# Kernel tuning notes

Measured on AMD Instinct MI355X. Metric: run time of the kernel, lower is better.

Reference implementation:

```python
import jax, jax.numpy as jnp
import numpy as np

H = 16  # n_heads (from init_kwargs)


def l2norm(x, eps=1e-6):
    return x * jax.lax.rsqrt(jnp.sum(x * x, axis=-1, keepdims=True) + eps)


def causal_conv1d(x, w, b):
    # depthwise causal conv: x (B,T,D), w (D,k), b (D,). Matches torch
    # Conv1d(d,d,k,groups=d,padding=k-1) followed by [:, :, :T] truncation.
    T = x.shape[1]
    k = w.shape[1]
    xp = jnp.pad(x, ((0, 0), (k - 1, 0), (0, 0)))
    y = b
    for j in range(k):  # k=4 taps, fixed small loop
        y = y + xp[:, j:j + T, :] * w[:, j]
    return y


def setup_inputs():
    key = jax.random.key(0)
    ks = jax.random.split(key, 16)
    B, T, D, kc = 2, 2048, 1024, 4
    d = D // H
    s = 1.0 / np.sqrt(D)
    return {
        "x": jax.random.normal(ks[0], (B, T, D), jnp.float32),
        "Wq": jax.random.normal(ks[1], (D, D), jnp.float32) * s,
        "Wk": jax.random.normal(ks[2], (D, D), jnp.float32) * s,
        "Wv": jax.random.normal(ks[3], (D, D), jnp.float32) * s,
        "Wo": jax.random.normal(ks[4], (D, D), jnp.float32) * s,
        "Wg": jax.random.normal(ks[5], (D, D), jnp.float32) * s,
        "Wb": jax.random.normal(ks[6], (D, H), jnp.float32) * s,
        "cq_w": jax.random.normal(ks[7], (D, kc), jnp.float32) * 0.3,
        "cq_b": jax.random.normal(ks[8], (D,), jnp.float32) * 0.1,
        "ck_w": jax.random.normal(ks[9], (D, kc), jnp.float32) * 0.3,
        "ck_b": jax.random.normal(ks[10], (D,), jnp.float32) * 0.1,
        "cv_w": jax.random.normal(ks[11], (D, kc), jnp.float32) * 0.3,
        "cv_b": jax.random.normal(ks[12], (D,), jnp.float32) * 0.1,
        "nw": jnp.ones((d,), jnp.float32),
    }


def reference(x, Wq, Wk, Wv, Wo, Wg, Wb, cq_w, cq_b, ck_w, ck_b, cv_w, cv_b, nw):
    B, T, D = x.shape
    d = D // H
    q = l2norm(jax.nn.silu(causal_conv1d(x @ Wq, cq_w, cq_b)).reshape(B, T, H, d))
    q = q / jnp.sqrt(jnp.asarray(d, x.dtype))
    k = l2norm(jax.nn.silu(causal_conv1d(x @ Wk, ck_w, ck_b)).reshape(B, T, H, d))
    v = jax.nn.silu(causal_conv1d(x @ Wv, cv_w, cv_b)).reshape(B, T, H, d)
    gate = (x @ Wg).reshape(B, T, H, d)
    beta = jax.nn.sigmoid(x @ Wb)[..., None]  # (B,T,H,1)

    def step(S, qkvb):
        q_t, k_t, v_t, b_t = qkvb  # (B,H,d), (B,H,d), (B,H,d), (B,H,1)
        err = (v_t - jnp.einsum('bhk,bhkv->bhv', k_t, S)) * b_t
        S = S + jnp.einsum('bhk,bhv->bhkv', k_t, err)
        o_t = jnp.einsum('bhk,bhkv->bhv', q_t, S)
        return S, o_t

    S0 = jnp.zeros((B, H, d, d), x.dtype)
    xs = (q.transpose(1, 0, 2, 3), k.transpose(1, 0, 2, 3),
          v.transpose(1, 0, 2, 3), beta.transpose(1, 0, 2, 3))
    _, oT = jax.lax.scan(step, S0, xs)
    o = oT.transpose(1, 0, 2, 3)  # (B,T,H,d)
    # RMSNorm over head_dim
    o = o * jax.lax.rsqrt(jnp.mean(o * o, axis=-1, keepdims=True) + 1e-5) * nw
    o = o * jax.nn.silu(gate)
    return o.reshape(B, T, D) @ Wo
```

## Files before the change

kernel.cpp:

```cpp
#include <hip/hip_runtime.h>
#include <hip/hip_bf16.h>

typedef __attribute__((ext_vector_type(8))) short short8;
typedef __attribute__((ext_vector_type(4))) float f32x4;

#define TSEQ 2048
#define DMODEL 1024
#define NH 16
#define HD 64
#define PLANE 4194304

__device__ __forceinline__ ushort f2bf(float f) {
    union { float f; unsigned int u; } c; c.f = f;
    unsigned int u = c.u + 0x7fffu + ((c.u >> 16) & 1u);
    return (ushort)(u >> 16);
}

__device__ __forceinline__ float bf2f(ushort u) {
    union { unsigned int i; float f; } c; c.i = ((unsigned int)u) << 16;
    return c.f;
}

__device__ __forceinline__ void split2(float x, ushort& h, ushort& l) {
    h = f2bf(x);
    float r = x - bf2f(h);
    l = f2bf(r);
}

__device__ __forceinline__ float silu_f(float y) {
    return y / (1.f + __expf(-y));
}

__device__ __forceinline__ void gl_lds16(const float* g, float* l) {
    __builtin_amdgcn_global_load_lds(
        (__attribute__((address_space(1))) void*)g,
        (__attribute__((address_space(3))) void*)l, 16, 0, 0);
}
__device__ __forceinline__ void gl_lds16u(const ushort* g, ushort* l) {
    __builtin_amdgcn_global_load_lds(
        (__attribute__((address_space(1))) void*)g,
        (__attribute__((address_space(3))) void*)l, 16, 0, 0);
}

__global__ void gdn_cvt_x(const float* __restrict__ x, ushort* __restrict__ xb) {
    int i = blockIdx.x * 256 + threadIdx.x;
    float4 v = ((const float4*)x)[i];
    ushort4 o;
    o.x = f2bf(v.x); o.y = f2bf(v.y); o.z = f2bf(v.z); o.w = f2bf(v.w);
    ((ushort4*)xb)[i] = o;
}

__global__ void gdn_cvt_w(const float* __restrict__ Wq, const float* __restrict__ Wk,
                          const float* __restrict__ Wv, const float* __restrict__ Wg,
                          const float* __restrict__ Wo, ushort* __restrict__ wt) {
    __shared__ float tile[32][33];
    int z = blockIdx.z;
    const float* W = (z == 0) ? Wq : (z == 1) ? Wk : (z == 2) ? Wv : (z == 3) ? Wg : Wo;
    int n0 = blockIdx.x * 32, k0 = blockIdx.y * 32;
    int tx = threadIdx.x, ty = threadIdx.y;
    #pragma unroll
    for (int j = 0; j < 32; j += 8)
        tile[ty + j][tx] = W[(size_t)(k0 + ty + j) * DMODEL + n0 + tx];
    __syncthreads();
    ushort* o = wt + (size_t)z * DMODEL * DMODEL;
    #pragma unroll
    for (int j = 0; j < 32; j += 8)
        o[(size_t)(n0 + ty + j) * DMODEL + k0 + tx] = f2bf(tile[tx][ty + j]);
}

__global__ void gdn_beta(const float* __restrict__ x, const float* __restrict__ Wb,
                         float* __restrict__ betaT) {
    __shared__ float xs[16][DMODEL];
    int tid = threadIdx.x;
    int m0 = blockIdx.x * 16;
    #pragma unroll
    for (int i = 0; i < 16; i++) {
        int idx = i * 256 + tid;
        int row = idx >> 8, c4 = idx & 255;
        *(float4*)&xs[row][c4 * 4] =
            *(const float4*)&x[(size_t)(m0 + row) * DMODEL + c4 * 4];
    }
    __syncthreads();
    int h = tid & 15, mi = tid >> 4;
    float acc = 0.f;
    for (int k = 0; k < DMODEL; ++k)
        acc += xs[mi][k] * Wb[k * NH + h];
    int m = m0 + mi;
    int b = m >> 11, t = m & (TSEQ - 1);
    betaT[((b * NH + h) << 11) + t] = 1.f / (1.f + __expf(-acc));
}

#define BK 32
__global__ __launch_bounds__(256) void gdn_gemm(const ushort* __restrict__ A,
                                                const ushort* __restrict__ Bt,
                                                float* __restrict__ outF,
                                                size_t planeStride) {
    __shared__ ushort As[128 * BK];
    __shared__ ushort Bs[128 * BK];
    int tid = threadIdx.x;
    int lane = tid & 63, wid = tid >> 6;
    int wm = wid & 1, wn = wid >> 1;
    int l15 = lane & 15, quad = lane >> 4;
    int bm = blockIdx.x, bn = blockIdx.y;
    const int K = DMODEL;

    int e0 = wid, e1 = wid + 4;
    int srow0 = e0 * 16 + (lane >> 2), srow1 = e1 * 16 + (lane >> 2);
    int scol = (lane & 3) * 8;
    const ushort* Ag0 = A + (size_t)(bm * 128 + srow0) * K + scol;
    const ushort* Ag1 = A + (size_t)(bm * 128 + srow1) * K + scol;
    const ushort* Bg0 = Bt + (size_t)(bn * 128 + srow0) * K + scol;
    const ushort* Bg1 = Bt + (size_t)(bn * 128 + srow1) * K + scol;
    ushort* Al0 = As + e0 * 512;
    ushort* Al1 = As + e1 * 512;
    ushort* Bl0 = Bs + e0 * 512;
    ushort* Bl1 = Bs + e1 * 512;

    f32x4 acc[4][4];
    #pragma unroll
    for (int i = 0; i < 4; i++)
        #pragma unroll
        for (int j = 0; j < 4; j++)
            acc[i][j] = (f32x4){0.f, 0.f, 0.f, 0.f};

    for (int kt = 0; kt < K; kt += BK) {
        __syncthreads();
        gl_lds16u(Ag0 + kt, Al0);
        gl_lds16u(Ag1 + kt, Al1);
        gl_lds16u(Bg0 + kt, Bl0);
        gl_lds16u(Bg1 + kt, Bl1);
        __syncthreads();
        short8 af[4], bf[4];
        #pragma unroll
        for (int i = 0; i < 4; i++) {
            af[i] = *(const short8*)&As[(wm * 64 + i * 16 + l15) * BK + quad * 8];
            bf[i] = *(const short8*)&Bs[(wn * 64 + i * 16 + l15) * BK + quad * 8];
        }
        #pragma unroll
        for (int mt = 0; mt < 4; mt++)
            #pragma unroll
            for (int nt = 0; nt < 4; nt++)
                acc[mt][nt] = __builtin_amdgcn_mfma_f32_16x16x32_bf16(
                    af[mt], bf[nt], acc[mt][nt], 0, 0, 0);
    }

    #pragma unroll
    for (int mt = 0; mt < 4; mt++)
        #pragma unroll
        for (int nt = 0; nt < 4; nt++)
            #pragma unroll
            for (int r = 0; r < 4; r++) {
                int row = bm * 128 + wm * 64 + mt * 16 + quad * 4 + r;
                int col = bn * 128 + wn * 64 + nt * 16 + l15;
                outF[(size_t)(col >> 10) * planeStride + (size_t)row * 1024 + (col & 1023)]
                    = acc[mt][nt][r];
            }
}

__global__ __launch_bounds__(512, 2) void gdn_gemm256(const ushort* __restrict__ A,
                                                      const ushort* __restrict__ Bt,
                                                      float* __restrict__ outF,
                                                      size_t planeStride) {
    __shared__ ushort As[3][256 * BK];
    __shared__ ushort Bs[3][256 * BK];
    int tid = threadIdx.x;
    int lane = tid & 63, wid = tid >> 6;
    int wm = wid >> 2, wn = wid & 3;
    int l15 = lane & 15, quad = lane >> 4;
    int bm = blockIdx.x, bn = blockIdx.y;
    const int K = DMODEL;

    int e0 = wid * 2, e1 = wid * 2 + 1;
    int srow0 = e0 * 16 + (lane >> 2), srow1 = e1 * 16 + (lane >> 2);
    int scol = (lane & 3) * 8;
    const ushort* Ag0 = A + (size_t)(bm * 256 + srow0) * K + scol;
    const ushort* Ag1 = A + (size_t)(bm * 256 + srow1) * K + scol;
    const ushort* Bg0 = Bt + (size_t)(bn * 256 + srow0) * K + scol;
    const ushort* Bg1 = Bt + (size_t)(bn * 256 + srow1) * K + scol;

    f32x4 acc[8][4];
    #pragma unroll
    for (int i = 0; i < 8; i++)
        #pragma unroll
        for (int j = 0; j < 4; j++)
            acc[i][j] = (f32x4){0.f, 0.f, 0.f, 0.f};

    #pragma unroll
    for (int t = 0; t < 2; t++) {
        gl_lds16u(Ag0 + t * BK, &As[t][e0 * 512]);
        gl_lds16u(Ag1 + t * BK, &As[t][e1 * 512]);
        gl_lds16u(Bg0 + t * BK, &Bs[t][e0 * 512]);
        gl_lds16u(Bg1 + t * BK, &Bs[t][e1 * 512]);
    }
    asm volatile("s_waitcnt vmcnt(4)" ::: "memory");
    __builtin_amdgcn_s_barrier();

    #pragma unroll 1
    for (int c = 0; c < 32; ++c) {
        if (c + 2 < 32) {
            int s2 = (c + 2) % 3;
            int kt2 = (c + 2) * BK;
            gl_lds16u(Ag0 + kt2, &As[s2][e0 * 512]);
            gl_lds16u(Ag1 + kt2, &As[s2][e1 * 512]);
            gl_lds16u(Bg0 + kt2, &Bs[s2][e0 * 512]);
            gl_lds16u(Bg1 + kt2, &Bs[s2][e1 * 512]);
        }
        int cs = c % 3;
        short8 af[8], bf[4];
        #pragma unroll
        for (int mi = 0; mi < 8; mi++)
            af[mi] = *(const short8*)&As[cs][(wm * 128 + mi * 16 + l15) * BK + quad * 8];
        #pragma unroll
        for (int ni = 0; ni < 4; ni++)
            bf[ni] = *(const short8*)&Bs[cs][(wn * 64 + ni * 16 + l15) * BK + quad * 8];
        #pragma unroll
        for (int mi = 0; mi < 8; mi++)
            #pragma unroll
            for (int ni = 0; ni < 4; ni++)
                acc[mi][ni] = __builtin_amdgcn_mfma_f32_16x16x32_bf16(
                    af[mi], bf[ni], acc[mi][ni], 0, 0, 0);
        if (c < 30) {
            asm volatile("s_waitcnt vmcnt(4)" ::: "memory");
            __builtin_amdgcn_s_barrier();
        } else if (c == 30) {
            asm volatile("s_waitcnt vmcnt(0)" ::: "memory");
            __builtin_amdgcn_s_barrier();
        }
    }

    #pragma unroll
    for (int mi = 0; mi < 8; mi++)
        #pragma unroll
        for (int ni = 0; ni < 4; ni++)
            #pragma unroll
            for (int r = 0; r < 4; r++) {
                int row = bm * 256 + wm * 128 + mi * 16 + quad * 4 + r;
                int col = bn * 256 + wn * 64 + ni * 16 + l15;
                outF[(size_t)(col >> 10) * planeStride + (size_t)row * 1024 + (col & 1023)]
                    = acc[mi][ni][r];
            }
}

__global__ void gdn_conv(const float* __restrict__ pre,
                         const float* __restrict__ cqw, const float* __restrict__ cqb,
                         const float* __restrict__ ckw, const float* __restrict__ ckb,
                         const float* __restrict__ cvw, const float* __restrict__ cvb,
                         float* __restrict__ qn, float* __restrict__ kn, float* __restrict__ vn) {
    int m = blockIdx.x;
    int which = blockIdx.y;
    int t = m & (TSEQ - 1);
    const float* cw = (which == 0) ? cqw : (which == 1) ? ckw : cvw;
    const float* cb = (which == 0) ? cqb : (which == 1) ? ckb : cvb;
    float* dst = (which == 0) ? qn : (which == 1) ? kn : vn;
    int c = threadIdx.x * 4;

    float w[4][4];
    #pragma unroll
    for (int i = 0; i < 4; i++) {
        float4 t4 = ((const float4*)cw)[c + i];
        w[i][0] = t4.x; w[i][1] = t4.y; w[i][2] = t4.z; w[i][3] = t4.w;
    }
    float4 bias = ((const float4*)cb)[threadIdx.x];
    float y[4] = {bias.x, bias.y, bias.z, bias.w};

    const float* src = pre + (size_t)which * PLANE + (size_t)m * DMODEL + c;
    #pragma unroll
    for (int j = 0; j < 4; j++) {
        int tt = t - 3 + j;
        if (tt >= 0) {
            float4 xv = *(const float4*)(src + (long)(j - 3) * DMODEL);
            y[0] += xv.x * w[0][j];
            y[1] += xv.y * w[1][j];
            y[2] += xv.z * w[2][j];
            y[3] += xv.w * w[3][j];
        }
    }
    #pragma unroll
    for (int i = 0; i < 4; i++) y[i] = silu_f(y[i]);

    if (which < 2) {
        float ss = y[0]*y[0] + y[1]*y[1] + y[2]*y[2] + y[3]*y[3];
        ss += __shfl_xor(ss, 1);
        ss += __shfl_xor(ss, 2);
        ss += __shfl_xor(ss, 4);
        ss += __shfl_xor(ss, 8);
        float sc = rsqrtf(ss + 1e-6f);
        if (which == 0) sc *= 0.125f;
        #pragma unroll
        for (int i = 0; i < 4; i++) y[i] *= sc;
    }
    float4 o; o.x = y[0]; o.y = y[1]; o.z = y[2]; o.w = y[3];
    ((float4*)(dst + (size_t)m * 1024))[threadIdx.x] = o;
}

__global__ __launch_bounds__(256, 2) void gdn_chunk(
    const float* __restrict__ kn, const float* __restrict__ vn,
    const float* __restrict__ betaT,
    ushort* __restrict__ WTst, ushort* __restrict__ U0st,
    float* __restrict__ Pst, float* __restrict__ Rst)
{
    __shared__ __align__(16) ushort bufA[2 * 4608];
    __shared__ __align__(16) ushort bufKT[2 * 4608];
    __shared__ __align__(16) ushort XThi[128 * 72];
    __shared__ __align__(16) ushort XTlo[128 * 72];
    __shared__ float bet[64];

    ushort* Khi    = bufA;          ushort* Klo    = bufA + 4608;
    ushort* Mneghi = bufA;          ushort* Mneglo = bufA + 4608;
    ushort* KThi   = bufKT;         ushort* KTlo   = bufKT + 4608;
    float*  Xs     = (float*)bufKT;
    float*  MmDiag = (float*)(bufKT + 4608);

    int c = blockIdx.x, bh = blockIdx.y;
    int b = bh >> 4, h = bh & 15;
    int tid = threadIdx.x;
    int w = tid >> 6, lane = tid & 63;
    int l15 = lane & 15, quad = lane >> 4;
    size_t gbase = ((size_t)(b * TSEQ + c * 64)) * DMODEL + h * 64;
    size_t u = (size_t)bh * 32 + c;

    if (tid < 64) bet[tid] = betaT[((size_t)bh << 11) + c * 64 + tid];
    #pragma unroll
    for (int i = 0; i < 18; i++) {
        ((uint*)XThi)[tid + 256 * i] = 0u;
        ((uint*)XTlo)[tid + 256 * i] = 0u;
    }
    #pragma unroll
    for (int i = 0; i < 4; i++) {
        int idx = tid + 256 * i;
        int r = idx >> 4, c4 = (idx & 15) * 4;
        float4 kv = *(const float4*)&kn[gbase + (size_t)r * DMODEL + c4];
        ushort h0, l0, h1, l1, h2, l2, h3, l3;
        split2(kv.x, h0, l0); split2(kv.y, h1, l1);
        split2(kv.z, h2, l2); split2(kv.w, h3, l3);
        ((uint*)&Khi[r * 72 + c4])[0] = (uint)h0 | ((uint)h1 << 16);
        ((uint*)&Khi[r * 72 + c4])[1] = (uint)h2 | ((uint)h3 << 16);
        ((uint*)&Klo[r * 72 + c4])[0] = (uint)l0 | ((uint)l1 << 16);
        ((uint*)&Klo[r * 72 + c4])[1] = (uint)l2 | ((uint)l3 << 16);
    }
    __syncthreads();

    {
        f32x4 mAcc[4];
        #pragma unroll
        for (int tn = 0; tn < 4; tn++) mAcc[tn] = (f32x4){0.f, 0.f, 0.f, 0.f};
        #pragma unroll
        for (int ks = 0; ks < 2; ks++) {
            short8 aH = *(const short8*)&Khi[(16 * w + l15) * 72 + ks * 32 + quad * 8];
            short8 aL = *(const short8*)&Klo[(16 * w + l15) * 72 + ks * 32 + quad * 8];
            #pragma unroll
            for (int tn = 0; tn < 4; tn++) {
                short8 bH = *(const short8*)&Khi[(16 * tn + l15) * 72 + ks * 32 + quad * 8];
                short8 bL = *(const short8*)&Klo[(16 * tn + l15) * 72 + ks * 32 + quad * 8];
                mAcc[tn] = __builtin_amdgcn_mfma_f32_16x16x32_bf16(aH, bH, mAcc[tn], 0, 0, 0);
                mAcc[tn] = __builtin_amdgcn_mfma_f32_16x16x32_bf16(aH, bL, mAcc[tn], 0, 0, 0);
                mAcc[tn] = __builtin_amdgcn_mfma_f32_16x16x32_bf16(aL, bH, mAcc[tn], 0, 0, 0);
            }
        }
        __syncthreads();
        #pragma unroll
        for (int tn = 0; tn < 4; tn++) {
            #pragma unroll
            for (int r = 0; r < 4; r++) {
                int row = 16 * w + quad * 4 + r;
                int col = tn * 16 + l15;
                float val = mAcc[tn][r] * bet[row];
                ushort hh = 0, ll = 0;
                if (col < row) {
                    float nv = -val;
                    hh = f2bf(nv);
                    ll = f2bf(nv - bf2f(hh));
                }
                Mneghi[row * 72 + col] = hh;
                Mneglo[row * 72 + col] = ll;
                if (tn == w) MmDiag[w * 320 + (row & 15) * 20 + l15] = val;
            }
        }
    }
    __syncthreads();

    #pragma unroll 1
    for (int st = 0; st < 4; st++) {
        int tb = st * 16;
        {
            int rl = tid >> 4, c4 = (tid & 15) * 4;
            int r = tb + rl;
            float br = bet[r];
            float4 kv = *(const float4*)&kn[gbase + (size_t)r * DMODEL + c4];
            float4 vv = *(const float4*)&vn[gbase + (size_t)r * DMODEL + c4];
            float4 xk; xk.x = br * kv.x; xk.y = br * kv.y; xk.z = br * kv.z; xk.w = br * kv.w;
            float4 xv; xv.x = br * vv.x; xv.y = br * vv.y; xv.z = br * vv.z; xv.w = br * vv.w;
            *(float4*)&Xs[rl * 132 + c4] = xk;
            *(float4*)&Xs[rl * 132 + 64 + c4] = xv;
        }
        __syncthreads();

        if (st) {
            f32x4 acc2[2];
            #pragma unroll
            for (int e = 0; e < 2; e++) {
                int tn = 2 * w + e;
                #pragma unroll
                for (int r = 0; r < 4; r++)
                    acc2[e][r] = Xs[(quad * 4 + r) * 132 + tn * 16 + l15];
            }
            #pragma unroll
            for (int ks = 0; ks < 2; ks++) {
                short8 aH = *(const short8*)&Mneghi[(tb + l15) * 72 + ks * 32 + quad * 8];
                short8 aL = *(const short8*)&Mneglo[(tb + l15) * 72 + ks * 32 + quad * 8];
                #pragma unroll
                for (int e = 0; e < 2; e++) {
                    int tn = 2 * w + e;
                    short8 bH = *(const short8*)&XThi[(tn * 16 + l15) * 72 + ks * 32 + quad * 8];
                    short8 bL = *(const short8*)&XTlo[(tn * 16 + l15) * 72 + ks * 32 + quad * 8];
                    acc2[e] = __builtin_amdgcn_mfma_f32_16x16x32_bf16(aH, bH, acc2[e], 0, 0, 0);
                    acc2[e] = __builtin_amdgcn_mfma_f32_16x16x32_bf16(aH, bL, acc2[e], 0, 0, 0);
                    acc2[e] = __builtin_amdgcn_mfma_f32_16x16x32_bf16(aL, bH, acc2[e], 0, 0, 0);
                }
            }
            #pragma unroll
            for (int e = 0; e < 2; e++) {
                int tn = 2 * w + e;
                #pragma unroll
                for (int r = 0; r < 4; r++)
                    Xs[(quad * 4 + r) * 132 + tn * 16 + l15] = acc2[e][r];
            }
            __syncthreads();
        }

        if (tid < 128) {
            const int j = tid;
            const float* MD = &MmDiag[st * 320];
            float xr[16];
            #pragma unroll
            for (int sb = 0; sb < 4; sb++) {
                float b4[4];
                #pragma unroll
                for (int i = 0; i < 4; i++)
                    b4[i] = Xs[(sb * 4 + i) * 132 + j];
                #pragma unroll
                for (int u4 = 0; u4 < sb; u4++) {
                    #pragma unroll
                    for (int i = 0; i < 4; i++) {
                        float4 m4 = *(const float4*)&MD[(sb * 4 + i) * 20 + u4 * 4];
                        b4[i] -= m4.x * xr[u4 * 4 + 0] + m4.y * xr[u4 * 4 + 1]
                               + m4.z * xr[u4 * 4 + 2] + m4.w * xr[u4 * 4 + 3];
                    }
                }
                float x0 = b4[0];
                float x1 = b4[1] - MD[(sb * 4 + 1) * 20 + sb * 4 + 0] * x0;
                float x2 = b4[2] - MD[(sb * 4 + 2) * 20 + sb * 4 + 0] * x0
                                 - MD[(sb * 4 + 2) * 20 + sb * 4 + 1] * x1;
                float x3 = b4[3] - MD[(sb * 4 + 3) * 20 + sb * 4 + 0] * x0
                                 - MD[(sb * 4 + 3) * 20 + sb * 4 + 1] * x1
                                 - MD[(sb * 4 + 3) * 20 + sb * 4 + 2] * x2;
                xr[sb * 4 + 0] = x0; xr[sb * 4 + 1] = x1;
                xr[sb * 4 + 2] = x2; xr[sb * 4 + 3] = x3;
            }
            ushort hs[16], ls[16];
            #pragma unroll
            for (int i = 0; i < 16; i++) split2(xr[i], hs[i], ls[i]);
            uint4 ph0, ph1, pl0, pl1;
            ph0.x = (uint)hs[0] | ((uint)hs[1] << 16);  ph0.y = (uint)hs[2] | ((uint)hs[3] << 16);
            ph0.z = (uint)hs[4] | ((uint)hs[5] << 16);  ph0.w = (uint)hs[6] | ((uint)hs[7] << 16);
            ph1.x = (uint)hs[8] | ((uint)hs[9] << 16);  ph1.y = (uint)hs[10] | ((uint)hs[11] << 16);
            ph1.z = (uint)hs[12] | ((uint)hs[13] << 16); ph1.w = (uint)hs[14] | ((uint)hs[15] << 16);
            pl0.x = (uint)ls[0] | ((uint)ls[1] << 16);  pl0.y = (uint)ls[2] | ((uint)ls[3] << 16);
            pl0.z = (uint)ls[4] | ((uint)ls[5] << 16);  pl0.w = (uint)ls[6] | ((uint)ls[7] << 16);
            pl1.x = (uint)ls[8] | ((uint)ls[9] << 16);  pl1.y = (uint)ls[10] | ((uint)ls[11] << 16);
            pl1.z = (uint)ls[12] | ((uint)ls[13] << 16); pl1.w = (uint)ls[14] | ((uint)ls[15] << 16);
            *(uint4*)&XThi[j * 72 + tb] = ph0;  *(uint4*)&XThi[j * 72 + tb + 8] = ph1;
            *(uint4*)&XTlo[j * 72 + tb] = pl0;  *(uint4*)&XTlo[j * 72 + tb + 8] = pl1;
            if (j < 64) {
                ushort* wdst = WTst + u * 4096 + j * 64 + tb;
                *(uint4*)wdst = ph0; *(uint4*)(wdst + 8) = ph1;
            } else {
                ushort* udst = U0st + u * 4096 + (size_t)tb * 64 + (j - 64);
                #pragma unroll
                for (int i = 0; i < 16; i++) udst[i * 64] = hs[i];
            }
        }
        __syncthreads();
    }

    #pragma unroll
    for (int i = 0; i < 4; i++) {
        int idx = tid + 256 * i;
        int r = idx >> 4, c4 = (idx & 15) * 4;
        float4 kv = *(const float4*)&kn[gbase + (size_t)r * DMODEL + c4];
        ushort h0, l0, h1, l1, h2, l2, h3, l3;
        split2(kv.x, h0, l0); split2(kv.y, h1, l1);
        split2(kv.z, h2, l2); split2(kv.w, h3, l3);
        KThi[(c4 + 0) * 72 + r] = h0; KThi[(c4 + 1) * 72 + r] = h1;
        KThi[(c4 + 2) * 72 + r] = h2; KThi[(c4 + 3) * 72 + r] = h3;
        KTlo[(c4 + 0) * 72 + r] = l0; KTlo[(c4 + 1) * 72 + r] = l1;
        KTlo[(c4 + 2) * 72 + r] = l2; KTlo[(c4 + 3) * 72 + r] = l3;
    }
    __syncthreads();

    {
        f32x4 pAcc[4], rAcc[4];
        #pragma unroll
        for (int tn = 0; tn < 4; tn++) {
            pAcc[tn] = (f32x4){0.f, 0.f, 0.f, 0.f};
            rAcc[tn] = (f32x4){0.f, 0.f, 0.f, 0.f};
        }
        #pragma unroll
        for (int ks = 0; ks < 2; ks++) {
            short8 aH = *(const short8*)&XThi[(16 * w + l15) * 72 + ks * 32 + quad * 8];
            short8 aL = *(const short8*)&XTlo[(16 * w + l15) * 72 + ks * 32 + quad * 8];
            short8 cH = *(const short8*)&KThi[(16 * w + l15) * 72 + ks * 32 + quad * 8];
            short8 cL = *(const short8*)&KTlo[(16 * w + l15) * 72 + ks * 32 + quad * 8];
            #pragma unroll
            for (int tn = 0; tn < 4; tn++) {
                short8 bH = *(const short8*)&KThi[(16 * tn + l15) * 72 + ks * 32 + quad * 8];
                short8 bL = *(const short8*)&KTlo[(16 * tn + l15) * 72 + ks * 32 + quad * 8];
                pAcc[tn] = __builtin_amdgcn_mfma_f32_16x16x32_bf16(aH, bH, pAcc[tn], 0, 0, 0);
                pAcc[tn] = __builtin_amdgcn_mfma_f32_16x16x32_bf16(aH, bL, pAcc[tn], 0, 0, 0);
                pAcc[tn] = __builtin_amdgcn_mfma_f32_16x16x32_bf16(aL, bH, pAcc[tn], 0, 0, 0);
                short8 uH = *(const short8*)&XThi[(64 + 16 * tn + l15) * 72 + ks * 32 + quad * 8];
                short8 uL = *(const short8*)&XTlo[(64 + 16 * tn + l15) * 72 + ks * 32 + quad * 8];
                rAcc[tn] = __builtin_amdgcn_mfma_f32_16x16x32_bf16(cH, uH, rAcc[tn], 0, 0, 0);
                rAcc[tn] = __builtin_amdgcn_mfma_f32_16x16x32_bf16(cH, uL, rAcc[tn], 0, 0, 0);
                rAcc[tn] = __builtin_amdgcn_mfma_f32_16x16x32_bf16(cL, uH, rAcc[tn], 0, 0, 0);
            }
        }
        float* Po = Pst + u * 4096;
        float* Ro = Rst + u * 4096;
        #pragma unroll
        for (int tn = 0; tn < 4; tn++) {
            #pragma unroll
            for (int r = 0; r < 4; r++) {
                int row = 16 * w + quad * 4 + r;
                int col = tn * 16 + l15;
                Po[row * 64 + col] = pAcc[tn][r];
                Ro[col * 64 + row] = rAcc[tn][r];
            }
        }
    }
}

__global__ __launch_bounds__(256) void gdn_sstep(const float* __restrict__ Pst,
                                                 const float* __restrict__ Rst,
                                                 float* __restrict__ S0st)
{
    __shared__ float PTl[3][4096];
    __shared__ float Rl[3][1024];
    __shared__ float SshT[2][16][72];

    int bh = blockIdx.x >> 2, cg = blockIdx.x & 3;
    int tid = threadIdx.x;
    int t0 = (tid & 15) * 4;
    int j  = tid >> 4;
    int jg = cg * 16 + j;
    int wv = tid >> 6, ln = tid & 63;

    size_t ubase = (size_t)bh * 32 * 4096;

    *(float4*)&SshT[0][j][t0] = (float4){0.f, 0.f, 0.f, 0.f};

    #pragma unroll
    for (int t = 0; t < 2; t++) {
        size_t ub = ubase + (size_t)t * 4096;
        #pragma unroll
        for (int q = 0; q < 4; q++)
            gl_lds16(Pst + ub + (wv * 4 + q) * 256 + ln * 4, &PTl[t][(wv * 4 + q) * 256]);
        gl_lds16(Rst + ub + cg * 1024 + wv * 256 + ln * 4, &Rl[t][wv * 256]);
    }
    asm volatile("s_waitcnt vmcnt(5)" ::: "memory");
    asm volatile("s_waitcnt lgkmcnt(0)" ::: "memory");
    __builtin_amdgcn_s_barrier();

    int cur3 = 0;
    #pragma unroll 1
    for (int c = 0; c < 32; ++c) {
        int cur = c & 1, nxt = cur ^ 1;
        if (c + 2 < 32) {
            int b3 = cur3 + 2; if (b3 >= 3) b3 -= 3;
            size_t ub2 = ubase + (size_t)(c + 2) * 4096;
            #pragma unroll
            for (int q = 0; q < 4; q++)
                gl_lds16(Pst + ub2 + (wv * 4 + q) * 256 + ln * 4, &PTl[b3][(wv * 4 + q) * 256]);
            gl_lds16(Rst + ub2 + cg * 1024 + wv * 256 + ln * 4, &Rl[b3][wv * 256]);
        }
        float4 sold = *(const float4*)&SshT[cur][j][t0];
        size_t ub = ubase + (size_t)c * 4096;
        S0st[ub + (size_t)(t0 + 0) * 64 + jg] = sold.x;
        S0st[ub + (size_t)(t0 + 1) * 64 + jg] = sold.y;
        S0st[ub + (size_t)(t0 + 2) * 64 + jg] = sold.z;
        S0st[ub + (size_t)(t0 + 3) * 64 + jg] = sold.w;
        float4 racc = *(const float4*)&Rl[cur3][j * 64 + t0];
        float sub0 = 0.f, sub1 = 0.f, sub2 = 0.f, sub3 = 0.f;
        #pragma unroll
        for (int u4 = 0; u4 < 16; u4++) {
            float4 sv = *(const float4*)&SshT[cur][j][u4 * 4];
            #pragma unroll
            for (int e = 0; e < 4; e++) {
                float4 pt = *(const float4*)&PTl[cur3][(u4 * 4 + e) * 64 + t0];
                float s1 = (e == 0) ? sv.x : (e == 1) ? sv.y : (e == 2) ? sv.z : sv.w;
                sub0 = fmaf(pt.x, s1, sub0);
                sub1 = fmaf(pt.y, s1, sub1);
                sub2 = fmaf(pt.z, s1, sub2);
                sub3 = fmaf(pt.w, s1, sub3);
            }
        }
        float4 snew;
        snew.x = sold.x + racc.x - sub0;
        snew.y = sold.y + racc.y - sub1;
        snew.z = sold.z + racc.z - sub2;
        snew.w = sold.w + racc.w - sub3;
        *(float4*)&SshT[nxt][j][t0] = snew;
        if (c == 0)       { asm volatile("s_waitcnt vmcnt(9)"  ::: "memory"); }
        else if (c < 30)  { asm volatile("s_waitcnt vmcnt(13)" ::: "memory"); }
        else if (c == 30) { asm volatile("s_waitcnt vmcnt(8)"  ::: "memory"); }
        asm volatile("s_waitcnt lgkmcnt(0)" ::: "memory");
        __builtin_amdgcn_s_barrier();
        cur3 += 1; if (cur3 >= 3) cur3 -= 3;
    }
}

__global__ __launch_bounds__(256) void gdn_opass(
    const float* __restrict__ qn, const float* __restrict__ kn,
    const float* __restrict__ S0st, const ushort* __restrict__ WTst,
    const ushort* __restrict__ U0st, float* __restrict__ otmp2)
{
    __shared__ ushort pool[36864];
    ushort* Qhi  = pool;
    ushort* Qlo  = pool + 4608;
    ushort* Khi  = pool + 2 * 4608;
    ushort* Klo  = pool + 3 * 4608;
    ushort* SThi = pool + 4 * 4608;
    ushort* STlo = pool + 5 * 4608;
    ushort* Wn   = pool + 6 * 4608;
    ushort* Uu   = pool + 7 * 4608;
    ushort* Ghi  = Qhi;  ushort* Glo  = Qlo;
    ushort* EThi = Khi;  ushort* ETlo = Klo;

    int c = blockIdx.x, bh = blockIdx.y;
    int b = bh >> 4, h = bh & 15;
    int tid = threadIdx.x;
    int w = tid >> 6, lane = tid & 63;
    int l15 = lane & 15, quad = lane >> 4;
    size_t gbase = ((size_t)(b * TSEQ + c * 64)) * DMODEL + h * 64;
    size_t u = (size_t)bh * 32 + c;

    #pragma unroll
    for (int i = 0; i < 4; i++) {
        int idx = tid + 256 * i;
        int r = idx >> 4, c4 = (idx & 15) * 4;
        float4 qv = *(const float4*)&qn[gbase + (size_t)r * DMODEL + c4];
        float4 kv = *(const float4*)&kn[gbase + (size_t)r * DMODEL + c4];
        float4 sv = *(const float4*)&S0st[u * 4096 + (size_t)idx * 4];
        ushort h0, l0, h1, l1, h2, l2, h3, l3;
        split2(qv.x, h0, l0); split2(qv.y, h1, l1);
        split2(qv.z, h2, l2); split2(qv.w, h3, l3);
        ((uint*)&Qhi[r * 72 + c4])[0] = (uint)h0 | ((uint)h1 << 16);
        ((uint*)&Qhi[r * 72 + c4])[1] = (uint)h2 | ((uint)h3 << 16);
        ((uint*)&Qlo[r * 72 + c4])[0] = (uint)l0 | ((uint)l1 << 16);
        ((uint*)&Qlo[r * 72 + c4])[1] = (uint)l2 | ((uint)l3 << 16);
        split2(kv.x, h0, l0); split2(kv.y, h1, l1);
        split2(kv.z, h2, l2); split2(kv.w, h3, l3);
        ((uint*)&Khi[r * 72 + c4])[0] = (uint)h0 | ((uint)h1 << 16);
        ((uint*)&Khi[r * 72 + c4])[1] = (uint)h2 | ((uint)h3 << 16);
        ((uint*)&Klo[r * 72 + c4])[0] = (uint)l0 | ((uint)l1 << 16);
        ((uint*)&Klo[r * 72 + c4])[1] = (uint)l2 | ((uint)l3 << 16);
        split2(sv.x, h0, l0); split2(sv.y, h1, l1);
        split2(sv.z, h2, l2); split2(sv.w, h3, l3);
        SThi[(c4 + 0) * 72 + r] = h0; STlo[(c4 + 0) * 72 + r] = l0;
        SThi[(c4 + 1) * 72 + r] = h1; STlo[(c4 + 1) * 72 + r] = l1;
        SThi[(c4 + 2) * 72 + r] = h2; STlo[(c4 + 2) * 72 + r] = l2;
        SThi[(c4 + 3) * 72 + r] = h3; STlo[(c4 + 3) * 72 + r] = l3;
    }
    #pragma unroll
    for (int i = 0; i < 2; i++) {
        int idx = tid + 256 * i;
        uint4 w8 = ((const uint4*)(WTst + u * 4096))[idx];
        int ur = idx >> 3, t8 = (idx & 7) * 8;
        uint v0 = w8.x ^ 0x80008000u, v1 = w8.y ^ 0x80008000u;
        uint v2 = w8.z ^ 0x80008000u, v3 = w8.w ^ 0x80008000u;
        Wn[(t8 + 0) * 72 + ur] = (ushort)v0; Wn[(t8 + 1) * 72 + ur] = (ushort)(v0 >> 16);
        Wn[(t8 + 2) * 72 + ur] = (ushort)v1; Wn[(t8 + 3) * 72 + ur] = (ushort)(v1 >> 16);
        Wn[(t8 + 4) * 72 + ur] = (ushort)v2; Wn[(t8 + 5) * 72 + ur] = (ushort)(v2 >> 16);
        Wn[(t8 + 6) * 72 + ur] = (ushort)v3; Wn[(t8 + 7) * 72 + ur] = (ushort)(v3 >> 16);
        ((uint4*)Uu)[idx] = ((const uint4*)(U0st + u * 4096))[idx];
    }
    __syncthreads();

    f32x4 accG[4], accO[4], accE[4];
    #pragma unroll
    for (int tn = 0; tn < 4; tn++) {
        accG[tn] = (f32x4){0.f, 0.f, 0.f, 0.f};
        accO[tn] = (f32x4){0.f, 0.f, 0.f, 0.f};
        #pragma unroll
        for (int r = 0; r < 4; r++)
            accE[tn][r] = bf2f(Uu[(16 * w + quad * 4 + r) * 64 + tn * 16 + l15]);
    }
    #pragma unroll
    for (int ks = 0; ks < 2; ks++) {
        int ko = ks * 32 + quad * 8;
        short8 qH = *(const short8*)&Qhi[(16 * w + l15) * 72 + ko];
        short8 qL = *(const short8*)&Qlo[(16 * w + l15) * 72 + ko];
        short8 wA = *(const short8*)&Wn [(16 * w + l15) * 72 + ko];
        #pragma unroll
        for (int tn = 0; tn < 4; tn++) {
            short8 kH = *(const short8*)&Khi [(16 * tn + l15) * 72 + ko];
            short8 kL = *(const short8*)&Klo [(16 * tn + l15) * 72 + ko];
            short8 sH = *(const short8*)&SThi[(16 * tn + l15) * 72 + ko];
            short8 sL = *(const short8*)&STlo[(16 * tn + l15) * 72 + ko];
            accG[tn] = __builtin_amdgcn_mfma_f32_16x16x32_bf16(qH, kH, accG[tn], 0, 0, 0);
            accG[tn] = __builtin_amdgcn_mfma_f32_16x16x32_bf16(qH, kL, accG[tn], 0, 0, 0);
            accG[tn] = __builtin_amdgcn_mfma_f32_16x16x32_bf16(qL, kH, accG[tn], 0, 0, 0);
            accO[tn] = __builtin_amdgcn_mfma_f32_16x16x32_bf16(qH, sH, accO[tn], 0, 0, 0);
            accO[tn] = __builtin_amdgcn_mfma_f32_16x16x32_bf16(qH, sL, accO[tn], 0, 0, 0);
            accO[tn] = __builtin_amdgcn_mfma_f32_16x16x32_bf16(qL, sH, accO[tn], 0, 0, 0);
            accE[tn] = __builtin_amdgcn_mfma_f32_16x16x32_bf16(wA, sH, accE[tn], 0, 0, 0);
            accE[tn] = __builtin_amdgcn_mfma_f32_16x16x32_bf16(wA, sL, accE[tn], 0, 0, 0);
        }
    }
    __syncthreads();

    #pragma unroll
    for (int tn = 0; tn < 4; tn++) {
        #pragma unroll
        for (int r = 0; r < 4; r++) {
            int row = 16 * w + quad * 4 + r;
            int col = tn * 16 + l15;
            float gv = (col <= row) ? accG[tn][r] : 0.f;
            ushort gh, gl; split2(gv, gh, gl);
            Ghi[row * 72 + col] = gh; Glo[row * 72 + col] = gl;
            ushort eh, el; split2(accE[tn][r], eh, el);
            EThi[col * 72 + row] = eh; ETlo[col * 72 + row] = el;
        }
    }
    __syncthreads();

    #pragma unroll
    for (int ks = 0; ks < 2; ks++) {
        int ko = ks * 32 + quad * 8;
        short8 gH = *(const short8*)&Ghi[(16 * w + l15) * 72 + ko];
        short8 gL = *(const short8*)&Glo[(16 * w + l15) * 72 + ko];
        #pragma unroll
        for (int tn = 0; tn < 4; tn++) {
            short8 eH = *(const short8*)&EThi[(16 * tn + l15) * 72 + ko];
            short8 eL = *(const short8*)&ETlo[(16 * tn + l15) * 72 + ko];
            accO[tn] = __builtin_amdgcn_mfma_f32_16x16x32_bf16(gH, eH, accO[tn], 0, 0, 0);
            accO[tn] = __builtin_amdgcn_mfma_f32_16x16x32_bf16(gH, eL, accO[tn], 0, 0, 0);
            accO[tn] = __builtin_amdgcn_mfma_f32_16x16x32_bf16(gL, eH, accO[tn], 0, 0, 0);
        }
    }

    #pragma unroll
    for (int tn = 0; tn < 4; tn++) {
        #pragma unroll
        for (int r = 0; r < 4; r++) {
            int row = 16 * w + quad * 4 + r;
            int col = tn * 16 + l15;
            otmp2[(((size_t)bh * 16 + (col >> 2)) * TSEQ + c * 64 + row) * 4 + (col & 3)]
                = accO[tn][r];
        }
    }
}

__global__ void gdn_fuse(const float* __restrict__ otmp2, const float* __restrict__ pre,
                         const float* __restrict__ nw, ushort* __restrict__ ofused) {
    int m = blockIdx.x;
    int b = m >> 11, t = m & (TSEQ - 1);
    int tid = threadIdx.x;
    float4 o = ((const float4*)otmp2)[((size_t)((b * NH + (tid >> 4)) * 16 + (tid & 15))) * TSEQ + t];
    float ss = o.x*o.x + o.y*o.y + o.z*o.z + o.w*o.w;
    ss += __shfl_xor(ss, 1);
    ss += __shfl_xor(ss, 2);
    ss += __shfl_xor(ss, 4);
    ss += __shfl_xor(ss, 8);
    float r = rsqrtf(ss * (1.f / 64.f) + 1e-5f);
    float4 nwv = ((const float4*)nw)[tid & 15];
    float4 g = ((const float4*)(pre + 3 * (size_t)PLANE + (size_t)m * DMODEL))[tid];
    ushort4 out;
    out.x = f2bf(o.x * r * nwv.x * silu_f(g.x));
    out.y = f2bf(o.y * r * nwv.y * silu_f(g.y));
    out.z = f2bf(o.z * r * nwv.z * silu_f(g.z));
    out.w = f2bf(o.w * r * nwv.w * silu_f(g.w));
    ((ushort4*)ofused)[m * 256 + tid] = out;
}

extern "C" void kernel_launch(void* const* d_in, const int* in_sizes, int n_in,
                              void* d_out, int out_size, void* d_ws, size_t ws_size,
                              hipStream_t stream) {
    const float* x    = (const float*)d_in[0];
    const float* Wq   = (const float*)d_in[1];
    const float* Wk   = (const float*)d_in[2];
    const float* Wv   = (const float*)d_in[3];
    const float* Wo   = (const float*)d_in[4];
    const float* Wg   = (const float*)d_in[5];
    const float* Wb   = (const float*)d_in[6];
    const float* cq_w = (const float*)d_in[7];
    const float* cq_b = (const float*)d_in[8];
    const float* ck_w = (const float*)d_in[9];
    const float* ck_b = (const float*)d_in[10];
    const float* cv_w = (const float*)d_in[11];
    const float* cv_b = (const float*)d_in[12];
    const float* nw   = (const float*)d_in[13];

    char* ws = (char*)d_ws;
    ushort* xb     = (ushort*)(ws);
    ushort* wt     = (ushort*)(ws + 8388608);
    float*  pre    = (float*)(ws + 18874368);
    float*  qn     = (float*)(ws + 85983232);
    float*  kn     = (float*)(ws + 102760448);
    float*  vn     = (float*)(ws + 119537664);
    float*  betaT  = (float*)(ws + 136314880);
    float*  otmp2  = (float*)(ws + 136577024);
    ushort* ofused = (ushort*)(ws + 153354240);

    float*  Pst  = pre;
    float*  Rst  = pre + PLANE;
    float*  S0st = pre + 2 * PLANE;
    ushort* WTst = xb;
    ushort* U0st = ofused;

    gdn_cvt_x<<<4096, 256, 0, stream>>>(x, xb);
    gdn_cvt_w<<<dim3(32, 32, 5), dim3(32, 8), 0, stream>>>(Wq, Wk, Wv, Wg, Wo, wt);
    gdn_beta<<<256, 256, 0, stream>>>(x, Wb, betaT);
    gdn_gemm256<<<dim3(16, 16), 512, 0, stream>>>(xb, wt, pre, (size_t)PLANE);
    gdn_conv<<<dim3(4096, 3), 256, 0, stream>>>(pre, cq_w, cq_b, ck_w, ck_b, cv_w, cv_b,
                                                qn, kn, vn);
    gdn_chunk<<<dim3(32, 32), 256, 0, stream>>>(kn, vn, betaT, WTst, U0st, Pst, Rst);
    gdn_sstep<<<128, 256, 0, stream>>>(Pst, Rst, S0st);
    gdn_opass<<<dim3(32, 32), 256, 0, stream>>>(qn, kn, S0st, WTst, U0st, otmp2);
    gdn_fuse<<<4096, 256, 0, stream>>>(otmp2, pre, nw, ofused);
    gdn_gemm<<<dim3(32, 8), 256, 0, stream>>>(ofused, wt + 4 * 1024 * 1024,
                                              (float*)d_out, (size_t)0);
}
```

Baseline: 375.5 us.

## Restructure 256-tile GEMM mainloop into 4-phase ping-pong pipeline with BK=64

Replaces the triple-buffered BK=32 mainloop of the 256x256 GEMM with a double-buffered BK=64 loop split into four MFMA quadrants. Global-to-LDS loads for the next B tile and the A tile two steps ahead are interleaved between quadrants, and s_setprio raises wave priority around MFMA bursts. The goal is better overlap of memory traffic with matrix math and fewer loop iterations and barriers per K. In exchange it adds several barriers per iteration and relies on subtle buffer-reuse ordering. The A prefetch overwrites the buffer currently being read, which is only safe if all waves have finished reading it.

```diff
diff --git a/kernel.cpp b/kernel.cpp
--- a/kernel.cpp
+++ b/kernel.cpp
@@ -161,22 +161,20 @@
                                                       const ushort* __restrict__ Bt,
                                                       float* __restrict__ outF,
                                                       size_t planeStride) {
-    __shared__ ushort As[3][256 * BK];
-    __shared__ ushort Bs[3][256 * BK];
+    __shared__ ushort As[2][256 * 64];
+    __shared__ ushort Bs[2][256 * 64];
     int tid = threadIdx.x;
     int lane = tid & 63, wid = tid >> 6;
     int wm = wid >> 2, wn = wid & 3;
     int l15 = lane & 15, quad = lane >> 4;
     int bm = blockIdx.x, bn = blockIdx.y;
     const int K = DMODEL;
-
-    int e0 = wid * 2, e1 = wid * 2 + 1;
-    int srow0 = e0 * 16 + (lane >> 2), srow1 = e1 * 16 + (lane >> 2);
-    int scol = (lane & 3) * 8;
-    const ushort* Ag0 = A + (size_t)(bm * 256 + srow0) * K + scol;
-    const ushort* Ag1 = A + (size_t)(bm * 256 + srow1) * K + scol;
-    const ushort* Bg0 = Bt + (size_t)(bn * 256 + srow0) * K + scol;
-    const ushort* Bg1 = Bt + (size_t)(bn * 256 + srow1) * K + scol;
+    const int NT = K / 64;
+
+    int rsub = wid * 8 + (lane >> 3);
+    int ldst = wid * 512;
+    const ushort* Ag = A + (size_t)(bm * 256 + rsub) * K + (lane & 7) * 8;
+    const ushort* Bg = Bt + (size_t)(bn * 256 + rsub) * K + (lane & 7) * 8;
 
     f32x4 acc[8][4];
     #pragma unroll
@@ -186,46 +184,107 @@
             acc[i][j] = (f32x4){0.f, 0.f, 0.f, 0.f};
 
     #pragma unroll
-    for (int t = 0; t < 2; t++) {
-        gl_lds16u(Ag0 + t * BK, &As[t][e0 * 512]);
-        gl_lds16u(Ag1 + t * BK, &As[t][e1 * 512]);
-        gl_lds16u(Bg0 + t * BK, &Bs[t][e0 * 512]);
-        gl_lds16u(Bg1 + t * BK, &Bs[t][e1 * 512]);
-    }
+    for (int g = 0; g < 4; g++)
+        gl_lds16u(Ag + (size_t)g * 64 * K, &As[0][g * 4096 + ldst]);
+    #pragma unroll
+    for (int g = 0; g < 4; g++)
+        gl_lds16u(Bg + (size_t)g * 64 * K, &Bs[0][g * 4096 + ldst]);
+    #pragma unroll
+    for (int g = 0; g < 4; g++)
+        gl_lds16u(Ag + (size_t)g * 64 * K + 64, &As[1][g * 4096 + ldst]);
     asm volatile("s_waitcnt vmcnt(4)" ::: "memory");
     __builtin_amdgcn_s_barrier();
 
     #pragma unroll 1
-    for (int c = 0; c < 32; ++c) {
-        if (c + 2 < 32) {
-            int s2 = (c + 2) % 3;
-            int kt2 = (c + 2) * BK;
-            gl_lds16u(Ag0 + kt2, &As[s2][e0 * 512]);
-            gl_lds16u(Ag1 + kt2, &As[s2][e1 * 512]);
-            gl_lds16u(Bg0 + kt2, &Bs[s2][e0 * 512]);
-            gl_lds16u(Bg1 + kt2, &Bs[s2][e1 * 512]);
-        }
-        int cs = c % 3;
-        short8 af[8], bf[4];
-        #pragma unroll
-        for (int mi = 0; mi < 8; mi++)
-            af[mi] = *(const short8*)&As[cs][(wm * 128 + mi * 16 + l15) * BK + quad * 8];
-        #pragma unroll
-        for (int ni = 0; ni < 4; ni++)
-            bf[ni] = *(const short8*)&Bs[cs][(wn * 64 + ni * 16 + l15) * BK + quad * 8];
-        #pragma unroll
-        for (int mi = 0; mi < 8; mi++)
-            #pragma unroll
-            for (int ni = 0; ni < 4; ni++)
-                acc[mi][ni] = __builtin_amdgcn_mfma_f32_16x16x32_bf16(
-                    af[mi], bf[ni], acc[mi][ni], 0, 0, 0);
-        if (c < 30) {
-            asm volatile("s_waitcnt vmcnt(4)" ::: "memory");
-            __builtin_amdgcn_s_barrier();
-        } else if (c == 30) {
-            asm volatile("s_waitcnt vmcnt(0)" ::: "memory");
-            __builtin_amdgcn_s_barrier();
-        }
+    for (int s = 0; s < 16; ++s) {
+        const ushort* Asb = As[s & 1];
+        const ushort* Bsb = Bs[s & 1];
+        int arow = wm * 128 + l15;
+        int brow = wn * 64 + l15;
+        short8 af[4][2], bf[4][2];
+
+        #pragma unroll
+        for (int i = 0; i < 4; i++) {
+            af[i][0] = *(const short8*)&Asb[(arow + i * 16) * 64 + quad * 8];
+            af[i][1] = *(const short8*)&Asb[(arow + i * 16) * 64 + 32 + quad * 8];
+        }
+        #pragma unroll
+        for (int j = 0; j < 2; j++) {
+            bf[j][0] = *(const short8*)&Bsb[(brow + j * 16) * 64 + quad * 8];
+            bf[j][1] = *(const short8*)&Bsb[(brow + j * 16) * 64 + 32 + quad * 8];
+        }
+        if (s + 1 < NT) {
+            gl_lds16u(Bg + (size_t)0 * 64 * K + (s + 1) * 64, &Bs[(s + 1) & 1][0 * 4096 + ldst]);
+            gl_lds16u(Bg + (size_t)1 * 64 * K + (s + 1) * 64, &Bs[(s + 1) & 1][1 * 4096 + ldst]);
+        }
+        __builtin_amdgcn_s_barrier();
+        __builtin_amdgcn_s_setprio(1);
+        #pragma unroll
+        for (int i = 0; i < 4; i++)
+            #pragma unroll
+            for (int j = 0; j < 2; j++) {
+                acc[i][j] = __builtin_amdgcn_mfma_f32_16x16x32_bf16(af[i][0], bf[j][0], acc[i][j], 0, 0, 0);
+                acc[i][j] = __builtin_amdgcn_mfma_f32_16x16x32_bf16(af[i][1], bf[j][1], acc[i][j], 0, 0, 0);
+            }
+        __builtin_amdgcn_s_setprio(0);
+        __builtin_amdgcn_s_barrier();
+
+        #pragma unroll
+        for (int j = 0; j < 2; j++) {
+            bf[2 + j][0] = *(const short8*)&Bsb[(brow + (2 + j) * 16) * 64 + quad * 8];
+            bf[2 + j][1] = *(const short8*)&Bsb[(brow + (2 + j) * 16) * 64 + 32 + quad * 8];
+        }
+        if (s + 1 < NT) {
+            gl_lds16u(Bg + (size_t)2 * 64 * K + (s + 1) * 64, &Bs[(s + 1) & 1][2 * 4096 + ldst]);
+            gl_lds16u(Bg + (size_t)3 * 64 * K + (s + 1) * 64, &Bs[(s + 1) & 1][3 * 4096 + ldst]);
+        }
+        __builtin_amdgcn_s_barrier();
+        __builtin_amdgcn_s_setprio(1);
+        #pragma unroll
+        for (int i = 0; i < 4; i++)
+            #pragma unroll
+            for (int j = 0; j < 2; j++) {
+                acc[i][2 + j] = __builtin_amdgcn_mfma_f32_16x16x32_bf16(af[i][0], bf[2 + j][0], acc[i][2 + j], 0, 0, 0);
+                acc[i][2 + j] = __builtin_amdgcn_mfma_f32_16x16x32_bf16(af[i][1], bf[2 + j][1], acc[i][2 + j], 0, 0, 0);
+            }
+        __builtin_amdgcn_s_setprio(0);
+        __builtin_amdgcn_s_barrier();
+
+        #pragma unroll
+        for (int i = 0; i < 4; i++) {
+            af[i][0] = *(const short8*)&Asb[(arow + 64 + i * 16) * 64 + quad * 8];
+            af[i][1] = *(const short8*)&Asb[(arow + 64 + i * 16) * 64 + 32 + quad * 8];
+        }
+        __builtin_amdgcn_s_barrier();
+        __builtin_amdgcn_s_setprio(1);
+        #pragma unroll
+        for (int i = 0; i < 4; i++)
+            #pragma unroll
+            for (int j = 0; j < 2; j++) {
+                acc[4 + i][j] = __builtin_amdgcn_mfma_f32_16x16x32_bf16(af[i][0], bf[j][0], acc[4 + i][j], 0, 0, 0);
+                acc[4 + i][j] = __builtin_amdgcn_mfma_f32_16x16x32_bf16(af[i][1], bf[j][1], acc[4 + i][j], 0, 0, 0);
+            }
+        __builtin_amdgcn_s_setprio(0);
+        __builtin_amdgcn_s_barrier();
+
+        if (s + 2 < NT) {
+            #pragma unroll
+            for (int g = 0; g < 4; g++)
+                gl_lds16u(Ag + (size_t)g * 64 * K + (s + 2) * 64, &As[s & 1][g * 4096 + ldst]);
+        }
+        __builtin_amdgcn_s_barrier();
+        __builtin_amdgcn_s_setprio(1);
+        #pragma unroll
+        for (int i = 0; i < 4; i++)
+            #pragma unroll
+            for (int j = 0; j < 2; j++) {
+                acc[4 + i][2 + j] = __builtin_amdgcn_mfma_f32_16x16x32_bf16(af[i][0], bf[2 + j][0], acc[4 + i][2 + j], 0, 0, 0);
+                acc[4 + i][2 + j] = __builtin_amdgcn_mfma_f32_16x16x32_bf16(af[i][1], bf[2 + j][1], acc[4 + i][2 + j], 0, 0, 0);
+            }
+        __builtin_amdgcn_s_setprio(0);
+        if (s < NT - 2)      { asm volatile("s_waitcnt vmcnt(4)" ::: "memory"); }
+        else if (s == NT - 2){ asm volatile("s_waitcnt vmcnt(0)" ::: "memory"); }
+        if (s < NT - 1) __builtin_amdgcn_s_barrier();
     }
 
     #pragma unroll
```

After: 377.6 us. Within noise of the previous version (+0.6%).
